# Kernel tuning notes

Measured on AMD Instinct MI355X. Metric: run time of the kernel, lower is better.

Reference implementation:

```python
import jax, jax.numpy as jnp
import numpy as np


def setup_inputs() -> dict:
    key = jax.random.key(0)
    ks = jax.random.split(key, 12)
    B, VIS, BOT, CTX, H, MLP_H = 256, 1024, 64, 512, 16, 4
    return {
        "x": jax.random.normal(ks[0], (B, VIS), jnp.float32),
        "reduce_w": jax.random.normal(ks[1], (VIS, BOT), jnp.float32) * 0.03,
        "reduce_b": jax.random.normal(ks[2], (BOT,), jnp.float32) * 0.01,
        "ann_w1": jax.random.normal(ks[3], (BOT, MLP_H), jnp.float32) * 0.1,
        "ann_b1": jax.random.normal(ks[4], (MLP_H,), jnp.float32) * 0.01,
        "ann_w2": jax.random.normal(ks[5], (MLP_H, CTX), jnp.float32) * 0.1,
        "ann_b2": jax.random.normal(ks[6], (CTX,), jnp.float32) * 0.01,
        "kan_W1": jax.random.normal(ks[7], (BOT, CTX, H), jnp.float32),
        "kan_b1": jnp.zeros((BOT, CTX, H), jnp.float32),
        "kan_W2": jax.random.normal(ks[8], (BOT, CTX, H), jnp.float32),
        "kan_b2": jnp.zeros((BOT, CTX), jnp.float32),
        "gate_w": jax.random.normal(ks[9], (BOT, CTX), jnp.float32) * 0.1,
        "gate_b": jax.random.normal(ks[10], (CTX,), jnp.float32) * 0.01,
    }


def reference(x, reduce_w, reduce_b, ann_w1, ann_b1, ann_w2, ann_b2,
              kan_W1, kan_b1, kan_W2, kan_b2, gate_w, gate_b):
    # reduce: (B, vis) -> (B, bot)
    z = x @ reduce_w + reduce_b
    # ANN branch: Linear -> ReLU -> Linear
    ann_out = jax.nn.relu(z @ ann_w1 + ann_b1) @ ann_w2 + ann_b2  # (B, ctx)
    # KAN branch: broadcast (B, in, out, hidden) chain fused into one expression
    h = jax.nn.relu(z[:, :, None, None] * kan_W1 + kan_b1)        # (B, in, out, H)
    kan_out = jnp.einsum('bioh,ioh->bo', h, kan_W2) + kan_b2.sum(axis=0)  # (B, ctx)
    # sigmoid gate on (z + 1)
    g = jax.nn.sigmoid((z + 1.0) @ gate_w + gate_b)               # (B, ctx)
    return g * ann_out + (1.0 - g) * kan_out
```

## Files before the change

kernel.cpp:

```cpp
#include <hip/hip_runtime.h>
#include <hip/hip_bf16.h>
#include <math.h>

#define B_SZ   256
#define VIS    1024
#define BOT    64
#define CTX    512
#define KH     16
#define MLP_H  4

__global__ __launch_bounds__(256) void kA(
    const float* __restrict__ x,
    const float* __restrict__ rw,
    const float* __restrict__ rb,
    const float* __restrict__ aw1,
    const float* __restrict__ ab1,
    const float* __restrict__ kb2,
    const float* __restrict__ gw,
    float* __restrict__ zT,
    float* __restrict__ a4,
    float* __restrict__ kb2s,
    float* __restrict__ gwsum)
{
    const int t = threadIdx.x;

    if (blockIdx.x >= B_SZ) {
        __shared__ float r0[4][64], r1[4][64];
        const int blk = blockIdx.x - B_SZ;
        const int w = t >> 6, l = t & 63;
        const int o = blk * 64 + l;
        float s0 = 0.f, s1 = 0.f;
#pragma unroll
        for (int ii = 0; ii < 16; ++ii) {
            const int i = w * 16 + ii;
            s0 += kb2[i * CTX + o];
            s1 += gw[i * CTX + o];
        }
        r0[w][l] = s0; r1[w][l] = s1;
        __syncthreads();
        if (t < 64) {
            kb2s[blk * 64 + t]  = r0[0][t] + r0[1][t] + r0[2][t] + r0[3][t];
            gwsum[blk * 64 + t] = r1[0][t] + r1[1][t] + r1[2][t] + r1[3][t];
        }
        return;
    }

    const int b  = blockIdx.x;
    const int w  = t >> 6, l = t & 63;
    const int kq = l >> 4, jq = l & 15;
    const int kbase = w * 256 + kq * 64;

    const float*  __restrict__ xb = x + (size_t)b * VIS + kbase;
    const float4* __restrict__ wb = (const float4*)rw + (size_t)kbase * 16 + jq;

    float4 a = make_float4(0.f, 0.f, 0.f, 0.f);
#pragma unroll 8
    for (int tt = 0; tt < 64; ++tt) {
        const float  xv = xb[tt];
        const float4 wv = wb[(size_t)tt * 16];
        a.x = fmaf(xv, wv.x, a.x);
        a.y = fmaf(xv, wv.y, a.y);
        a.z = fmaf(xv, wv.z, a.z);
        a.w = fmaf(xv, wv.w, a.w);
    }
    a.x += __shfl_xor(a.x, 16, 64); a.y += __shfl_xor(a.y, 16, 64);
    a.z += __shfl_xor(a.z, 16, 64); a.w += __shfl_xor(a.w, 16, 64);
    a.x += __shfl_xor(a.x, 32, 64); a.y += __shfl_xor(a.y, 32, 64);
    a.z += __shfl_xor(a.z, 32, 64); a.w += __shfl_xor(a.w, 32, 64);

    __shared__ float4 zp[4][16];
    __shared__ float  zs[64];
    if (l < 16) zp[w][jq] = a;
    __syncthreads();

    if (t < BOT) {
        const float* z0 = (const float*)&zp[0][0];
        const float z = z0[t] + z0[64 + t] + z0[128 + t] + z0[192 + t] + rb[t];
        zs[t] = z;
        zT[(size_t)t * B_SZ + b] = z;
    }
    __syncthreads();

    if (t < MLP_H) {
        float s = ab1[t];
#pragma unroll
        for (int i = 0; i < BOT; ++i) s = fmaf(zs[i], aw1[i * MLP_H + t], s);
        a4[b * MLP_H + t] = fmaxf(s, 0.f);
    }
}

__global__ __launch_bounds__(256) void k2_main(
    const float* __restrict__ zT,
    const float* __restrict__ a4,
    const float* __restrict__ aw2,
    const float* __restrict__ ab2,
    const float* __restrict__ kW1,
    const float* __restrict__ kb1,
    const float* __restrict__ kW2,
    const float* __restrict__ gw,
    const float* __restrict__ gb,
    const float* __restrict__ kb2s,
    const float* __restrict__ gwsum,
    float* __restrict__ out)
{
    __shared__ float pK[4][4][16][20];
    __shared__ float pG[4][16][20];

    const int t    = threadIdx.x;
    const int w    = t >> 6;
    const int lane = t & 63;
    const int o_l  = lane >> 2;
    const int hq   = lane & 3;
    const int o0   = blockIdx.x * 16;
    const int b0   = blockIdx.y * 16;

    float4 acc[16];
    float  accG[16];
#pragma unroll
    for (int b = 0; b < 16; ++b) {
        acc[b] = make_float4(0.f, 0.f, 0.f, 0.f);
        accG[b] = 0.f;
    }

    const int i0 = w * 16;
#pragma unroll 2
    for (int ii = 0; ii < 16; ++ii) {
        const int i = i0 + ii;
        const size_t wbo = ((size_t)i * CTX + o0) * KH + (size_t)lane * 4;
        const float4 w1 = *(const float4*)(kW1 + wbo);
        const float4 b1 = *(const float4*)(kb1 + wbo);
        const float4 w2 = *(const float4*)(kW2 + wbo);
        const float  gwv = gw[i * CTX + o0 + o_l];
        const float* __restrict__ zp = zT + (size_t)i * B_SZ + b0;
#pragma unroll
        for (int b = 0; b < 16; ++b) {
            const float z = zp[b];
            float4 hv;
            hv.x = fmaxf(fmaf(z, w1.x, b1.x), 0.f);
            hv.y = fmaxf(fmaf(z, w1.y, b1.y), 0.f);
            hv.z = fmaxf(fmaf(z, w1.z, b1.z), 0.f);
            hv.w = fmaxf(fmaf(z, w1.w, b1.w), 0.f);
            acc[b].x = fmaf(hv.x, w2.x, acc[b].x);
            acc[b].y = fmaf(hv.y, w2.y, acc[b].y);
            acc[b].z = fmaf(hv.z, w2.z, acc[b].z);
            acc[b].w = fmaf(hv.w, w2.w, acc[b].w);
            accG[b]  = fmaf(z, gwv, accG[b]);
        }
    }

    float aK[16];
#pragma unroll
    for (int b = 0; b < 16; ++b)
        aK[b] = (acc[b].x + acc[b].y) + (acc[b].z + acc[b].w);

    {
        float* d = &pK[w][hq][o_l][0];
        ((float4*)d)[0] = make_float4(aK[0],  aK[1],  aK[2],  aK[3]);
        ((float4*)d)[1] = make_float4(aK[4],  aK[5],  aK[6],  aK[7]);
        ((float4*)d)[2] = make_float4(aK[8],  aK[9],  aK[10], aK[11]);
        ((float4*)d)[3] = make_float4(aK[12], aK[13], aK[14], aK[15]);
    }
    if (hq == 0) {
        float* d = &pG[w][o_l][0];
        ((float4*)d)[0] = make_float4(accG[0],  accG[1],  accG[2],  accG[3]);
        ((float4*)d)[1] = make_float4(accG[4],  accG[5],  accG[6],  accG[7]);
        ((float4*)d)[2] = make_float4(accG[8],  accG[9],  accG[10], accG[11]);
        ((float4*)d)[3] = make_float4(accG[12], accG[13], accG[14], accG[15]);
    }
    __syncthreads();

    {
        const int o = t & 15;
        const int b = t >> 4;
        float sK = 0.f, sG = 0.f;
#pragma unroll
        for (int w2 = 0; w2 < 4; ++w2) {
#pragma unroll
            for (int h2 = 0; h2 < 4; ++h2)
                sK += pK[w2][h2][o][b];
            sG += pG[w2][o][b];
        }
        const int oo = o0 + o;
        const int bb = b0 + b;
        sK += kb2s[oo];
        sG += gwsum[oo] + gb[oo];

        const float4 av = *(const float4*)(a4 + bb * MLP_H);
        float ann = ab2[oo];
        ann = fmaf(av.x, aw2[0 * CTX + oo], ann);
        ann = fmaf(av.y, aw2[1 * CTX + oo], ann);
        ann = fmaf(av.z, aw2[2 * CTX + oo], ann);
        ann = fmaf(av.w, aw2[3 * CTX + oo], ann);

        const float g = 1.f / (1.f + __expf(-sG));
        out[(size_t)bb * CTX + oo] = g * ann + (1.f - g) * sK;
    }
}

extern "C" void kernel_launch(void* const* d_in, const int* in_sizes, int n_in,
                              void* d_out, int out_size, void* d_ws, size_t ws_size,
                              hipStream_t stream)
{
    const float* x   = (const float*)d_in[0];
    const float* rw  = (const float*)d_in[1];
    const float* rb  = (const float*)d_in[2];
    const float* aw1 = (const float*)d_in[3];
    const float* ab1 = (const float*)d_in[4];
    const float* aw2 = (const float*)d_in[5];
    const float* ab2 = (const float*)d_in[6];
    const float* kW1 = (const float*)d_in[7];
    const float* kb1 = (const float*)d_in[8];
    const float* kW2 = (const float*)d_in[9];
    const float* kb2 = (const float*)d_in[10];
    const float* gw  = (const float*)d_in[11];
    const float* gb  = (const float*)d_in[12];
    float* out = (float*)d_out;

    float* zT    = (float*)d_ws;
    float* a4    = zT + (size_t)BOT * B_SZ;
    float* kb2s  = a4 + (size_t)B_SZ * MLP_H;
    float* gwsum = kb2s + CTX;

    kA<<<B_SZ + 8, 256, 0, stream>>>(x, rw, rb, aw1, ab1, kb2, gw,
                                     zT, a4, kb2s, gwsum);
    k2_main<<<dim3(CTX / 16, B_SZ / 16), 256, 0, stream>>>(
        zT, a4, aw2, ab2, kW1, kb1, kW2, gw, gb, kb2s, gwsum, out);
}
```

Measured before the change: 101.0 us.

## Double block sizes, stage z in LDS, move gate and bias sums to epilogue

Both kernels go from 256 to 512 threads. Each wave now covers half as many input rows (8 instead of 16 in k2_main, 32 instead of 64 VIS elements in kA), so there are more waves in flight. k2_main stages the block's z tile in shared memory and drops the per-iteration gate accumulation. The gate matmul and the kb2 column sum are recomputed in the epilogue by 256 threads looping over 64 rows, and the 8 helper blocks that precomputed those sums in kA are removed. The hq partial reduction now uses wave shuffles instead of extra LDS traffic. The cost is redundant gw and kb2 reads in every block's epilogue, paid in exchange for more parallelism in the main loop.

```diff
diff --git a/kernel.cpp b/kernel.cpp
--- a/kernel.cpp
+++ b/kernel.cpp
@@ -9,53 +9,27 @@
 #define KH     16
 #define MLP_H  4
 
-__global__ __launch_bounds__(256) void kA(
+__global__ __launch_bounds__(512) void kA(
     const float* __restrict__ x,
     const float* __restrict__ rw,
     const float* __restrict__ rb,
     const float* __restrict__ aw1,
     const float* __restrict__ ab1,
-    const float* __restrict__ kb2,
-    const float* __restrict__ gw,
     float* __restrict__ zT,
-    float* __restrict__ a4,
-    float* __restrict__ kb2s,
-    float* __restrict__ gwsum)
+    float* __restrict__ a4)
 {
+    const int b = blockIdx.x;
     const int t = threadIdx.x;
-
-    if (blockIdx.x >= B_SZ) {
-        __shared__ float r0[4][64], r1[4][64];
-        const int blk = blockIdx.x - B_SZ;
-        const int w = t >> 6, l = t & 63;
-        const int o = blk * 64 + l;
-        float s0 = 0.f, s1 = 0.f;
-#pragma unroll
-        for (int ii = 0; ii < 16; ++ii) {
-            const int i = w * 16 + ii;
-            s0 += kb2[i * CTX + o];
-            s1 += gw[i * CTX + o];
-        }
-        r0[w][l] = s0; r1[w][l] = s1;
-        __syncthreads();
-        if (t < 64) {
-            kb2s[blk * 64 + t]  = r0[0][t] + r0[1][t] + r0[2][t] + r0[3][t];
-            gwsum[blk * 64 + t] = r1[0][t] + r1[1][t] + r1[2][t] + r1[3][t];
-        }
-        return;
-    }
-
-    const int b  = blockIdx.x;
-    const int w  = t >> 6, l = t & 63;
+    const int w = t >> 6, l = t & 63;
     const int kq = l >> 4, jq = l & 15;
-    const int kbase = w * 256 + kq * 64;
+    const int kbase = w * 128 + kq * 32;
 
     const float*  __restrict__ xb = x + (size_t)b * VIS + kbase;
     const float4* __restrict__ wb = (const float4*)rw + (size_t)kbase * 16 + jq;
 
     float4 a = make_float4(0.f, 0.f, 0.f, 0.f);
 #pragma unroll 8
-    for (int tt = 0; tt < 64; ++tt) {
+    for (int tt = 0; tt < 32; ++tt) {
         const float  xv = xb[tt];
         const float4 wv = wb[(size_t)tt * 16];
         a.x = fmaf(xv, wv.x, a.x);
@@ -68,14 +42,16 @@
     a.x += __shfl_xor(a.x, 32, 64); a.y += __shfl_xor(a.y, 32, 64);
     a.z += __shfl_xor(a.z, 32, 64); a.w += __shfl_xor(a.w, 32, 64);
 
-    __shared__ float4 zp[4][16];
+    __shared__ float4 zp[8][16];
     __shared__ float  zs[64];
     if (l < 16) zp[w][jq] = a;
     __syncthreads();
 
     if (t < BOT) {
         const float* z0 = (const float*)&zp[0][0];
-        const float z = z0[t] + z0[64 + t] + z0[128 + t] + z0[192 + t] + rb[t];
+        float z = rb[t];
+#pragma unroll
+        for (int wq = 0; wq < 8; ++wq) z += z0[wq * 64 + t];
         zs[t] = z;
         zT[(size_t)t * B_SZ + b] = z;
     }
@@ -89,7 +65,7 @@
     }
 }
 
-__global__ __launch_bounds__(256) void k2_main(
+__global__ __launch_bounds__(512) void k2_main(
     const float* __restrict__ zT,
     const float* __restrict__ a4,
     const float* __restrict__ aw2,
@@ -97,14 +73,13 @@
     const float* __restrict__ kW1,
     const float* __restrict__ kb1,
     const float* __restrict__ kW2,
+    const float* __restrict__ kb2,
     const float* __restrict__ gw,
     const float* __restrict__ gb,
-    const float* __restrict__ kb2s,
-    const float* __restrict__ gwsum,
     float* __restrict__ out)
 {
-    __shared__ float pK[4][4][16][20];
-    __shared__ float pG[4][16][20];
+    __shared__ float zl[BOT][16];
+    __shared__ float pK[8][16][24];
 
     const int t    = threadIdx.x;
     const int w    = t >> 6;
@@ -114,27 +89,32 @@
     const int o0   = blockIdx.x * 16;
     const int b0   = blockIdx.y * 16;
 
+    if (t < 256) {
+        const int i = t >> 2, q = t & 3;
+        ((float4*)&zl[i][0])[q] =
+            ((const float4*)(zT + (size_t)i * B_SZ + b0))[q];
+    }
+    __syncthreads();
+
     float4 acc[16];
-    float  accG[16];
-#pragma unroll
-    for (int b = 0; b < 16; ++b) {
-        acc[b] = make_float4(0.f, 0.f, 0.f, 0.f);
-        accG[b] = 0.f;
-    }
-
-    const int i0 = w * 16;
+#pragma unroll
+    for (int b = 0; b < 16; ++b) acc[b] = make_float4(0.f, 0.f, 0.f, 0.f);
+
+    const int i0 = w * 8;
 #pragma unroll 2
-    for (int ii = 0; ii < 16; ++ii) {
+    for (int ii = 0; ii < 8; ++ii) {
         const int i = i0 + ii;
         const size_t wbo = ((size_t)i * CTX + o0) * KH + (size_t)lane * 4;
         const float4 w1 = *(const float4*)(kW1 + wbo);
         const float4 b1 = *(const float4*)(kb1 + wbo);
         const float4 w2 = *(const float4*)(kW2 + wbo);
-        const float  gwv = gw[i * CTX + o0 + o_l];
-        const float* __restrict__ zp = zT + (size_t)i * B_SZ + b0;
+        const float4* zr = (const float4*)&zl[i][0];
+        const float4 za = zr[0], zb = zr[1], zc = zr[2], zd = zr[3];
+        const float zv[16] = { za.x, za.y, za.z, za.w,  zb.x, zb.y, zb.z, zb.w,
+                               zc.x, zc.y, zc.z, zc.w,  zd.x, zd.y, zd.z, zd.w };
 #pragma unroll
         for (int b = 0; b < 16; ++b) {
-            const float z = zp[b];
+            const float z = zv[b];
             float4 hv;
             hv.x = fmaxf(fmaf(z, w1.x, b1.x), 0.f);
             hv.y = fmaxf(fmaf(z, w1.y, b1.y), 0.f);
@@ -144,46 +124,45 @@
             acc[b].y = fmaf(hv.y, w2.y, acc[b].y);
             acc[b].z = fmaf(hv.z, w2.z, acc[b].z);
             acc[b].w = fmaf(hv.w, w2.w, acc[b].w);
-            accG[b]  = fmaf(z, gwv, accG[b]);
         }
     }
 
     float aK[16];
 #pragma unroll
-    for (int b = 0; b < 16; ++b)
-        aK[b] = (acc[b].x + acc[b].y) + (acc[b].z + acc[b].w);
-
-    {
-        float* d = &pK[w][hq][o_l][0];
+    for (int b = 0; b < 16; ++b) {
+        float s = (acc[b].x + acc[b].y) + (acc[b].z + acc[b].w);
+        s += __shfl_xor(s, 1, 64);
+        s += __shfl_xor(s, 2, 64);
+        aK[b] = s;
+    }
+    if (hq == 0) {
+        float* d = &pK[w][o_l][0];
         ((float4*)d)[0] = make_float4(aK[0],  aK[1],  aK[2],  aK[3]);
         ((float4*)d)[1] = make_float4(aK[4],  aK[5],  aK[6],  aK[7]);
         ((float4*)d)[2] = make_float4(aK[8],  aK[9],  aK[10], aK[11]);
         ((float4*)d)[3] = make_float4(aK[12], aK[13], aK[14], aK[15]);
     }
-    if (hq == 0) {
-        float* d = &pG[w][o_l][0];
-        ((float4*)d)[0] = make_float4(accG[0],  accG[1],  accG[2],  accG[3]);
-        ((float4*)d)[1] = make_float4(accG[4],  accG[5],  accG[6],  accG[7]);
-        ((float4*)d)[2] = make_float4(accG[8],  accG[9],  accG[10], accG[11]);
-        ((float4*)d)[3] = make_float4(accG[12], accG[13], accG[14], accG[15]);
-    }
-    __syncthreads();
-
-    {
+    __syncthreads();
+
+    if (t < 256) {
         const int o = t & 15;
         const int b = t >> 4;
-        float sK = 0.f, sG = 0.f;
-#pragma unroll
-        for (int w2 = 0; w2 < 4; ++w2) {
-#pragma unroll
-            for (int h2 = 0; h2 < 4; ++h2)
-                sK += pK[w2][h2][o][b];
-            sG += pG[w2][o][b];
-        }
         const int oo = o0 + o;
         const int bb = b0 + b;
-        sK += kb2s[oo];
-        sG += gwsum[oo] + gb[oo];
+
+        float sK = 0.f;
+#pragma unroll
+        for (int w2 = 0; w2 < 8; ++w2) sK += pK[w2][o][b];
+
+        float sG = 0.f, sKB = 0.f;
+#pragma unroll 8
+        for (int i = 0; i < BOT; ++i) {
+            const float zi = zl[i][b];
+            sG  = fmaf(zi + 1.f, gw[i * CTX + oo], sG);
+            sKB += kb2[i * CTX + oo];
+        }
+        sK += sKB;
+        sG += gb[oo];
 
         const float4 av = *(const float4*)(a4 + bb * MLP_H);
         float ann = ab2[oo];
@@ -216,13 +195,10 @@
     const float* gb  = (const float*)d_in[12];
     float* out = (float*)d_out;
 
-    float* zT    = (float*)d_ws;
-    float* a4    = zT + (size_t)BOT * B_SZ;
-    float* kb2s  = a4 + (size_t)B_SZ * MLP_H;
-    float* gwsum = kb2s + CTX;
-
-    kA<<<B_SZ + 8, 256, 0, stream>>>(x, rw, rb, aw1, ab1, kb2, gw,
-                                     zT, a4, kb2s, gwsum);
-    k2_main<<<dim3(CTX / 16, B_SZ / 16), 256, 0, stream>>>(
-        zT, a4, aw2, ab2, kW1, kb1, kW2, gw, gb, kb2s, gwsum, out);
+    float* zT = (float*)d_ws;
+    float* a4 = zT + (size_t)BOT * B_SZ;
+
+    kA<<<B_SZ, 512, 0, stream>>>(x, rw, rb, aw1, ab1, zT, a4);
+    k2_main<<<dim3(CTX / 16, B_SZ / 16), 512, 0, stream>>>(
+        zT, a4, aw2, ab2, kW1, kb1, kW2, kb2, gw, gb, out);
 }
```

Result: no change. 101.6 us (+0.6%).
